# Kernel optimization log

Hardware: AMD Instinct MI355X
Metric: run time of the kernel (lower is better)

The kernel has to match this reference:

```python
import jax, jax.numpy as jnp
import numpy as np

DIM, H, D, B, L = 1024, 8, 64, 1, 256


def silu(v):
    return v * jax.nn.sigmoid(v)


def setup_inputs() -> dict:
    key = jax.random.key(0)
    ks = jax.random.split(key, 12)
    n = lambda i, shape, scale=1.0: jax.random.normal(ks[i], shape, dtype=jnp.float32) * scale
    return {
        "x": n(0, (B, L, DIM)),
        "hidden_real": n(1, (B, H, D)),
        "hidden_imag": n(2, (B, H, D)),
        "w_in1": n(3, (DIM, DIM), 1.0 / np.sqrt(DIM)),
        "b_in1": jnp.zeros((DIM,), jnp.float32),
        "w_in2": n(4, (DIM, H * D * 4), 1.0 / np.sqrt(DIM)),
        "b_in2": jnp.zeros((H * D * 4,), jnp.float32),
        "w_out1": n(5, (H * D * 2, DIM), 1.0 / np.sqrt(H * D * 2)),
        "b_out1": jnp.zeros((DIM,), jnp.float32),
        "w_out2": n(6, (DIM, DIM), 1.0 / np.sqrt(DIM)),
        "b_out2": jnp.zeros((DIM,), jnp.float32),
        "mat_v_real": n(7, (H, D, D)),
        "mat_v_imag": n(8, (H, D, D)),
    }


def reference(x, hidden_real, hidden_imag, w_in1, b_in1, w_in2, b_in2,
              w_out1, b_out1, w_out2, b_out2, mat_v_real, mat_v_imag):
    batch, slen, _ = x.shape
    t = silu(x @ w_in1 + b_in1)
    t = t @ w_in2 + b_in2                       # (B, L, 4*H*D)
    z = t.reshape(batch, slen, H, D, 2, 2)      # [..., {x,a}, {re,im}]
    xc = jax.lax.complex(z[..., 0, 0], z[..., 0, 1])   # (B, L, H, D) complex
    ac = jax.lax.complex(z[..., 1, 0], z[..., 1, 1])

    # normalize a: unit phase * sigmoid(log(|a|^2)) magnitude
    mag2 = ac.real * ac.real + ac.imag * ac.imag
    ac = ac * (jax.lax.rsqrt(mag2) * jax.nn.sigmoid(jnp.log(mag2)))

    a_ln = jnp.log(ac)                          # (B, L, H, D) complex
    al = jnp.transpose(a_ln, (0, 2, 3, 1))      # (B, H, D, L)

    # triu-broadcast + cumsum along cols == the FFT conv-with-ones in the original
    idx = jnp.arange(slen)
    triu = idx[:, None] <= idx[None, :]          # row i, col j: keep j >= i
    tri = jnp.where(triu, al[..., None, :], 0.0)  # (B, H, D, L, L)
    cum = jnp.cumsum(tri, axis=-1)               # cum[i, k] = sum_{j=i..k} a_ln[j]
    keep = (idx[:, None] - 1) <= idx[None, :]    # triu(diagonal=-1)
    c = jnp.where(keep, jnp.exp(cum), 0.0)       # c[i,k] = prod_{j=i..k} a[j]; c[i,i-1]=1

    V = jax.lax.complex(mat_v_real, mat_v_imag)  # (H, D, D)
    Vinv = jnp.linalg.inv(V)
    hidden = jax.lax.complex(hidden_real, hidden_imag)  # (B, H, D)

    x_roll = jnp.concatenate([hidden.astype(xc.dtype)[:, None], xc[:, :-1]], axis=1)
    u = jnp.einsum('hno,blho->blhn', Vinv, x_roll)       # V^{-1} applied per head
    h = jnp.einsum('bholm,blho->bmho', c, u)             # banded product-scan
    h = h.at[:, -1].add(jnp.einsum('hno,bho->bhn', Vinv, xc[:, -1]))
    h = jnp.einsum('hno,blho->blhn', V, h)               # back to V-basis

    hidden_next = h[:, -1]                                # (B, H, D) complex
    hr = jnp.stack([h.real, h.imag], axis=-1).reshape(batch, slen, H * D * 2)
    y = silu(hr @ w_out1 + b_out1)
    y = y @ w_out2 + b_out2
    return y, hidden_next
```

## Files before the change

### kernel.cpp

```cpp
#include <hip/hip_runtime.h>
#include <math.h>

#define DIMN 1024
#define NH 8
#define ND 64
#define LSEQ 256
#define HD 512

typedef __attribute__((ext_vector_type(8))) short short8;
typedef __attribute__((ext_vector_type(4))) float f32x4;

__device__ __forceinline__ float2 cmul(float2 a, float2 b){
    return make_float2(a.x*b.x - a.y*b.y, a.x*b.y + a.y*b.x);
}
__device__ __forceinline__ ushort f2bf(float f){
    union { float f; unsigned u; } v; v.f = f;
    unsigned r = v.u + 0x7FFF + ((v.u >> 16) & 1);
    return (ushort)(r >> 16);
}

#define ISTR 65
#define ASTR 40
#define BK 32

__device__ __forceinline__ void inv_gj_blocked(const float* __restrict__ Vr,
        const float* __restrict__ Vi, float2* __restrict__ Vinv,
        int h, int tid, float2* Mx){
    for (int idx = tid; idx < 4096; idx += 512){
        int i = idx >> 6, j = idx & 63;
        Mx[i*ISTR + j] = make_float2(Vr[h*4096 + idx], Vi[h*4096 + idx]);
    }
    __syncthreads();
    const int w = tid >> 6, l = tid & 63;
    const int rbase = w*8;
    for (int kb = 0; kb < 8; ++kb){
        const int k0 = kb*8;
        if (w == 0){
            float2 pr[8];
            #pragma unroll
            for (int m = 0; m < 8; ++m) pr[m] = Mx[l*ISTR + k0 + m];
            #pragma unroll
            for (int k = 0; k < 8; ++k){
                const int gk = k0 + k;
                float2 d; d.x = __shfl(pr[k].x, gk); d.y = __shfl(pr[k].y, gk);
                float im = 1.f/(d.x*d.x + d.y*d.y);
                float2 p = make_float2(d.x*im, -d.y*im);
                float2 spr[8];
                #pragma unroll
                for (int m = 0; m < 8; ++m){
                    float2 t; t.x = __shfl(pr[m].x, gk); t.y = __shfl(pr[m].y, gk);
                    spr[m] = (m == k) ? p : cmul(t, p);
                }
                float2 f = pr[k];
                if (l == gk){
                    #pragma unroll
                    for (int m = 0; m < 8; ++m) pr[m] = spr[m];
                } else {
                    #pragma unroll
                    for (int m = 0; m < 8; ++m){
                        float2 u = cmul(f, spr[m]);
                        if (m == k){ pr[m].x = -u.x;  pr[m].y = -u.y;  }
                        else       { pr[m].x -= u.x;  pr[m].y -= u.y;  }
                    }
                }
            }
            #pragma unroll
            for (int m = 0; m < 8; ++m) Mx[l*ISTR + k0 + m] = pr[m];
        }
        __syncthreads();
        float2 br[8];
        #pragma unroll
        for (int m = 0; m < 8; ++m) br[m] = Mx[(k0+m)*ISTR + l];
        __syncthreads();
        if (((unsigned)(l - k0)) >= 8u){
            #pragma unroll
            for (int rr = 0; rr < 8; ++rr){
                const int r = rbase + rr;
                float2 acc;
                if (((unsigned)(r - k0)) < 8u){ acc.x = 0.f; acc.y = 0.f; }
                else acc = Mx[r*ISTR + l];
                #pragma unroll
                for (int m = 0; m < 8; ++m){
                    float2 Pv = Mx[r*ISTR + k0 + m];
                    acc.x += Pv.x*br[m].x - Pv.y*br[m].y;
                    acc.y += Pv.x*br[m].y + Pv.y*br[m].x;
                }
                Mx[r*ISTR + l] = acc;
            }
        }
        __syncthreads();
    }
    for (int idx = tid; idx < 4096; idx += 512){
        int i = idx >> 6, j = idx & 63;
        Vinv[h*4096 + idx] = Mx[i*ISTR + j];
    }
}

__device__ __forceinline__ void w3eff_tile(const float* __restrict__ Vr,
        const float* __restrict__ Vi, const float* __restrict__ w3,
        ushort* __restrict__ W3bt, int t, int tid, float* lds){
    const int n0 = (t & 31)*32;
    const int c0 = (t >> 5)*32;
    const int h  = c0 >> 7;
    const int og0 = (c0 & 127) >> 1;
    float* Vbr = lds;
    float* Vbi = lds + 1024;
    float* Wb  = lds + 2048;
    for (int q = tid; q < 1024; q += 512){
        int dd = q >> 4, oo = q & 15;
        Vbr[q] = Vr[(h*64+dd)*64 + og0 + oo];
        Vbi[q] = Vi[(h*64+dd)*64 + og0 + oo];
    }
    for (int q = tid; q < 4096; q += 512){
        int row = q >> 5, nn = q & 31;
        Wb[q] = w3[(h*128 + row)*1024 + n0 + nn];
    }
    __syncthreads();
    const int nn = tid & 31, oo = tid >> 5;
    float ar = 0.f, ai = 0.f;
    #pragma unroll 8
    for (int dd = 0; dd < 64; ++dd){
        float vr = Vbr[dd*16 + oo], vi = Vbi[dd*16 + oo];
        float w0 = Wb[(dd*2)*32 + nn], w1v = Wb[(dd*2+1)*32 + nn];
        ar += vr*w0 + vi*w1v;
        ai += -vi*w0 + vr*w1v;
    }
    W3bt[(n0+nn)*1024 + c0 + oo*2 + 0] = f2bf(ar);
    W3bt[(n0+nn)*1024 + c0 + oo*2 + 1] = f2bf(ai);
}

__global__ __launch_bounds__(512) void prep_kernel(
        const float* __restrict__ x,
        const float* __restrict__ w1, const float* __restrict__ w2,
        const float* __restrict__ w3, const float* __restrict__ w4,
        const float* __restrict__ Vr, const float* __restrict__ Vi,
        ushort* __restrict__ x_bf,
        ushort* __restrict__ w1t, ushort* __restrict__ w2t,
        ushort* __restrict__ w4t, ushort* __restrict__ W3bt,
        float2* __restrict__ Vinv){
    __shared__ __align__(16) char lds_raw[33280];
    const int b = blockIdx.x;
    const int tid = threadIdx.x;
    const int half = tid >> 8;

    if (b < 8){
        inv_gj_blocked(Vr, Vi, Vinv, b, tid, (float2*)lds_raw);
        return;
    }
    int u = b - 8;
    if (u < 2048){
        const float* W; ushort* Wt; const int K = 1024; int N; int t;
        if (u < 512)      { W = w1; Wt = w1t; N = 1024; t = u*2 + half; }
        else if (u < 1536){ W = w2; Wt = w2t; N = 2048; t = (u-512)*2 + half; }
        else              { W = w4; Wt = w4t; N = 1024; t = (u-1536)*2 + half; }
        const int tiles_n = N >> 5;
        const int n0 = (t % tiles_n) * 32, k0 = (t / tiles_n) * 32;
        float* tile = (float*)lds_raw + half*(32*33);
        const int tx = tid & 31, ty = (tid >> 5) & 7;
        #pragma unroll
        for (int i = 0; i < 4; ++i)
            tile[(ty + i*8)*33 + tx] = W[(k0 + ty + i*8)*N + n0 + tx];
        __syncthreads();
        #pragma unroll
        for (int i = 0; i < 4; ++i){
            int r = ty + i*8;
            Wt[(n0 + r)*K + k0 + tx] = f2bf(tile[tx*33 + r]);
        }
        return;
    }
    u -= 2048;
    if (u < 64){
        const int base = (u*512 + tid)*2;
        #pragma unroll
        for (int j = 0; j < 2; ++j){
            float4 v = ((const float4*)x)[base + j];
            ushort4 uu; uu.x=f2bf(v.x); uu.y=f2bf(v.y); uu.z=f2bf(v.z); uu.w=f2bf(v.w);
            ((ushort4*)x_bf)[base + j] = uu;
        }
        return;
    }
    u -= 64;
    w3eff_tile(Vr, Vi, w3, W3bt, u, tid, (float*)lds_raw);
}

template<int ACT>
__global__ __launch_bounds__(64) void gemm_dt(const ushort* __restrict__ A,
                 const ushort* __restrict__ Bt, const float* __restrict__ bias,
                 float* __restrict__ Cf, ushort* __restrict__ Cb,
                 float2* __restrict__ XCo, float2* __restrict__ Ao,
                 int M, int N, int K,
                 const float* __restrict__ tVr, const float* __restrict__ tVi,
                 const float2* __restrict__ S255, float* __restrict__ out_tail,
                 int tail_n){
    const int nt = (M >> 5) * (N >> 5);
    const int b = blockIdx.x;
    if (ACT == 1 && out_tail != nullptr && b >= nt){
        const int l = threadIdx.x;
        for (int hn = l; hn < 512; hn += 64){
            const int h = hn >> 6;
            float2 acc2 = make_float2(0.f, 0.f);
            #pragma unroll 8
            for (int o = 0; o < 64; ++o){
                float2 v = make_float2(tVr[hn*64+o], tVi[hn*64+o]);
                float2 p = cmul(v, S255[h*64+o]);
                acc2.x += p.x; acc2.y += p.y;
            }
            if (tail_n >= 1024){
                out_tail[hn]       = acc2.x;
                out_tail[512 + hn] = acc2.y;
            } else if (tail_n >= 512){
                out_tail[hn] = acc2.x;
            }
        }
        return;
    }
    const int cpx = nt >> 3;
    const int t = (b & 7)*cpx + (b >> 3);
    const int tm = M >> 5;
    const int bm = (t % tm) * 32, bn = (t / tm) * 32;

    const int l = threadIdx.x;
    const int ml = l & 15, quad = l >> 4;
    const ushort* Ap = A  + (bm + ml)*K + quad*8;
    const ushort* Bp = Bt + (bn + ml)*K + quad*8;

    f32x4 acc[2][2];
    #pragma unroll
    for (int i=0;i<2;++i)
        #pragma unroll
        for (int j=0;j<2;++j) acc[i][j] = (f32x4){0.f,0.f,0.f,0.f};

    short8 ac[2], bc[2];
    ac[0] = *(const short8*)(Ap);
    ac[1] = *(const short8*)(Ap + 16*K);
    bc[0] = *(const short8*)(Bp);
    bc[1] = *(const short8*)(Bp + 16*K);

    #pragma unroll 4
    for (int k0 = 32; k0 < K; k0 += 32){
        short8 an[2], bn2[2];
        an[0]  = *(const short8*)(Ap + k0);
        an[1]  = *(const short8*)(Ap + 16*K + k0);
        bn2[0] = *(const short8*)(Bp + k0);
        bn2[1] = *(const short8*)(Bp + 16*K + k0);
        #pragma unroll
        for (int i=0;i<2;++i)
            #pragma unroll
            for (int j=0;j<2;++j)
                acc[i][j] = __builtin_amdgcn_mfma_f32_16x16x32_bf16(ac[i], bc[j], acc[i][j], 0,0,0);
        ac[0]=an[0]; ac[1]=an[1]; bc[0]=bn2[0]; bc[1]=bn2[1];
    }
    #pragma unroll
    for (int i=0;i<2;++i)
        #pragma unroll
        for (int j=0;j<2;++j)
            acc[i][j] = __builtin_amdgcn_mfma_f32_16x16x32_bf16(ac[i], bc[j], acc[i][j], 0,0,0);

    #pragma unroll
    for (int i=0;i<2;++i){
        #pragma unroll
        for (int j=0;j<2;++j){
            const int gcol = bn + j*16 + ml;
            const float bsv = bias[gcol];
            #pragma unroll
            for (int r=0;r<4;++r){
                const int grow = bm + i*16 + quad*4 + r;
                float val = acc[i][j][r] + bsv;
                if (ACT == 2){
                    float v1 = __shfl_down(val, 1);
                    float v2 = __shfl_down(val, 2);
                    float v3 = __shfl_down(val, 3);
                    if ((l & 3) == 0){
                        int hd = gcol >> 2;
                        XCo[grow*HD + hd] = make_float2(val, v1);
                        float m2 = v2*v2 + v3*v3;
                        float s = sqrtf(m2)/(1.f + m2);
                        Ao[grow*HD + hd] = make_float2(v2*s, v3*s);
                    }
                } else if (ACT == 1){
                    val *= 1.f/(1.f + expf(-val));
                    Cb[grow*N + gcol] = f2bf(val);
                } else {
                    Cf[grow*N + gcol] = val;
                }
            }
        }
    }
}

__global__ __launch_bounds__(512) void inv_kernel(const float* __restrict__ Vr,
                                                  const float* __restrict__ Vi,
                                                  float2* __restrict__ Vinv){
    __shared__ float2 Mx[64*ISTR];
    inv_gj_blocked(Vr, Vi, Vinv, blockIdx.x, threadIdx.x, Mx);
}

__global__ __launch_bounds__(256) void transpose_cvt(const float* __restrict__ W,
                 ushort* __restrict__ Wt, int K, int N){
    __shared__ float tile[32][33];
    const int n0 = blockIdx.x * 32, k0 = blockIdx.y * 32;
    const int tx = threadIdx.x & 31, ty = threadIdx.x >> 5;
    #pragma unroll
    for (int i = 0; i < 4; ++i)
        tile[ty + i*8][tx] = W[(k0 + ty + i*8)*N + n0 + tx];
    __syncthreads();
    #pragma unroll
    for (int i = 0; i < 4; ++i){
        int r = ty + i*8;
        Wt[(n0 + r)*K + k0 + tx] = f2bf(tile[tx][r]);
    }
}

__global__ __launch_bounds__(256) void cvt_bf16_kernel(const float* __restrict__ in,
                                 ushort* __restrict__ o, int n4){
    int i = blockIdx.x*256 + threadIdx.x;
    if (i < n4){
        float4 v = ((const float4*)in)[i];
        ushort4 u; u.x=f2bf(v.x); u.y=f2bf(v.y); u.z=f2bf(v.z); u.w=f2bf(v.w);
        ((ushort4*)o)[i] = u;
    }
}

#define BM 64
#define BN 64
template<int ACT>
__global__ __launch_bounds__(256) void gemm_bt(const ushort* __restrict__ A,
                 const ushort* __restrict__ Bt, const float* __restrict__ bias,
                 float* __restrict__ Cf, ushort* __restrict__ Cb,
                 float2* __restrict__ XCo, float2* __restrict__ Ao,
                 int M, int N, int K,
                 const float* __restrict__ tVr, const float* __restrict__ tVi,
                 const float2* __restrict__ S255, float* __restrict__ out_tail,
                 int tail_n){
    __shared__ ushort As[BM*ASTR];
    __shared__ ushort Bs[BN*ASTR];
    const int tid = threadIdx.x;
    const int bm = blockIdx.y * BM, bn = blockIdx.x * BN;
    const int wave = tid >> 6, l = tid & 63;
    const int wr = (wave >> 1) * 32, wc = (wave & 1) * 32;
    const int ml = l & 15, quad = l >> 4;

    if (ACT == 0 && out_tail != nullptr && blockIdx.x == 0 && blockIdx.y == 0){
        for (int hn = tid; hn < 512; hn += 256){
            int h = hn >> 6;
            float2 acc2 = make_float2(0.f, 0.f);
            #pragma unroll 8
            for (int o = 0; o < 64; ++o){
                float2 v = make_float2(tVr[hn*64+o], tVi[hn*64+o]);
                float2 p = cmul(v, S255[h*64+o]);
                acc2.x += p.x; acc2.y += p.y;
            }
            if (tail_n >= 1024){
                out_tail[hn]       = acc2.x;
                out_tail[512 + hn] = acc2.y;
            } else if (tail_n >= 512){
                out_tail[hn] = acc2.x;
            }
        }
    }

    f32x4 acc[2][2];
    #pragma unroll
    for (int i=0;i<2;++i)
        #pragma unroll
        for (int j=0;j<2;++j) acc[i][j] = (f32x4){0.f,0.f,0.f,0.f};
    const int c0r = tid >> 2;
    const int c0s = tid & 3;
    for (int k0 = 0; k0 < K; k0 += BK){
        uint4 av = *(const uint4*)&A [(bm + c0r)*K + k0 + c0s*8];
        uint4 bv = *(const uint4*)&Bt[(bn + c0r)*K + k0 + c0s*8];
        __syncthreads();
        *(uint4*)&As[c0r*ASTR + c0s*8] = av;
        *(uint4*)&Bs[c0r*ASTR + c0s*8] = bv;
        __syncthreads();
        short8 af[2], bfv[2];
        #pragma unroll
        for (int f=0; f<2; ++f){
            af[f]  = *(const short8*)&As[(wr + f*16 + ml)*ASTR + quad*8];
            bfv[f] = *(const short8*)&Bs[(wc + f*16 + ml)*ASTR + quad*8];
        }
        #pragma unroll
        for (int i=0;i<2;++i)
            #pragma unroll
            for (int j=0;j<2;++j)
                acc[i][j] = __builtin_amdgcn_mfma_f32_16x16x32_bf16(af[i], bfv[j], acc[i][j], 0,0,0);
    }
    #pragma unroll
    for (int i=0;i<2;++i){
        #pragma unroll
        for (int j=0;j<2;++j){
            const int gcol = bn + wc + j*16 + ml;
            const float bsv = bias[gcol];
            #pragma unroll
            for (int r=0;r<4;++r){
                const int grow = bm + wr + i*16 + quad*4 + r;
                float val = acc[i][j][r] + bsv;
                if (ACT == 2){
                    float v1 = __shfl_down(val, 1);
                    float v2 = __shfl_down(val, 2);
                    float v3 = __shfl_down(val, 3);
                    if ((l & 3) == 0){
                        int hd = gcol >> 2;
                        XCo[grow*HD + hd] = make_float2(val, v1);
                        float m2 = v2*v2 + v3*v3;
                        float s = sqrtf(m2)/(1.f + m2);
                        Ao[grow*HD + hd] = make_float2(v2*s, v3*s);
                    }
                } else if (ACT == 1){
                    val *= 1.f/(1.f + expf(-val));
                    Cb[grow*N + gcol] = f2bf(val);
                } else {
                    Cf[grow*N + gcol] = val;
                }
            }
        }
    }
}

__global__ __launch_bounds__(512) void upscan_kernel(const float2* __restrict__ Vinv,
        const float* __restrict__ hidr, const float* __restrict__ him,
        const float2* __restrict__ XC, const float2* __restrict__ Aseq,
        ushort* __restrict__ Sb, float2* __restrict__ S255){
    __shared__ float4 buf[2][2][LSEQ];
    __shared__ float2 vrow[2][64];
    __shared__ float2 inu[2];
    const int b = blockIdx.x;
    const int tid = threadIdx.x;
    const int g = tid >> 8, m = tid & 255;
    const int hn = b*2 + g;
    const int h = hn >> 6;
    if (m < 64) vrow[g][m] = Vinv[hn*64 + m];
    __syncthreads();
    float2 acc = make_float2(0.f, 0.f);
    const float2* xrow = &XC[m*HD + h*64];
    #pragma unroll 8
    for (int o=0;o<64;++o){
        float2 p = cmul(vrow[g][o], xrow[o]);
        acc.x += p.x; acc.y += p.y;
    }
    if (m == 0){
        float2 i0 = make_float2(0.f, 0.f);
        #pragma unroll 8
        for (int o=0;o<64;++o){
            float2 hv = make_float2(hidr[h*64+o], him[h*64+o]);
            float2 p = cmul(vrow[g][o], hv);
            i0.x += p.x; i0.y += p.y;
        }
        inu[g] = i0;
    }
    float2 a = Aseq[m*HD + hn];
    buf[0][g][m] = make_float4(a.x, a.y, acc.x, acc.y);
    __syncthreads();
    int pb = 0;
    #pragma unroll
    for (int d = 1; d < LSEQ; d <<= 1){
        float4 cur = buf[pb][g][m];
        float4 o2 = cur;
        if (m >= d){
            float4 prev = buf[pb][g][m-d];
            float2 cA = make_float2(cur.x, cur.y), cU = make_float2(cur.z, cur.w);
            float2 pA = make_float2(prev.x, prev.y), pU = make_float2(prev.z, prev.w);
            float2 nA = cmul(cA, pA);
            float2 nU = cmul(cA, pU);
            nU.x += cU.x; nU.y += cU.y;
            o2 = make_float4(nA.x, nA.y, nU.x, nU.y);
        }
        buf[pb^1][g][m] = o2;
        pb ^= 1;
        __syncthreads();
    }
    float4 t = buf[pb][g][m];
    float2 init = inu[g];
    float2 st = cmul(make_float2(t.x, t.y), init);
    st.x += t.z; st.y += t.w;
    Sb[m*DIMN + hn*2]   = f2bf(st.x);
    Sb[m*DIMN + hn*2+1] = f2bf(st.y);
    if (m == LSEQ-1) S255[hn] = st;
}

__global__ __launch_bounds__(256) void vmul_kernel(const float* __restrict__ Vr,
                            const float* __restrict__ Vi,
                            const float2* __restrict__ S, ushort* __restrict__ hrb,
                            float* __restrict__ out_tail, int tail_n){
    int g = blockIdx.x*256 + threadIdx.x;
    int m = g >> 9, hn = g & 511;
    int h = hn >> 6;
    const float* vr = &Vr[hn*64];
    const float* vi = &Vi[hn*64];
    const float2* srow = &S[m*HD + h*64];
    float2 acc = make_float2(0.f, 0.f);
    #pragma unroll 8
    for (int o=0;o<64;++o){
        float2 v = make_float2(vr[o], vi[o]);
        float2 p = cmul(v, srow[o]);
        acc.x += p.x; acc.y += p.y;
    }
    hrb[m*DIMN + hn*2]   = f2bf(acc.x);
    hrb[m*DIMN + hn*2+1] = f2bf(acc.y);
    if (m == LSEQ-1){
        if (tail_n >= 1024){
            out_tail[hn]       = acc.x;
            out_tail[512 + hn] = acc.y;
        } else if (tail_n >= 512){
            out_tail[hn] = acc.x;
        }
    }
}

__global__ __launch_bounds__(512) void upscan_f32_kernel(const float2* __restrict__ Vinv,
        const float* __restrict__ hidr, const float* __restrict__ him,
        const float2* __restrict__ XC, const float2* __restrict__ Aseq,
        float2* __restrict__ S){
    __shared__ float4 buf[2][2][LSEQ];
    __shared__ float2 vrow[2][64];
    __shared__ float2 inu[2];
    const int b = blockIdx.x;
    const int tid = threadIdx.x;
    const int g = tid >> 8, m = tid & 255;
    const int hn = b*2 + g;
    const int h = hn >> 6;
    if (m < 64) vrow[g][m] = Vinv[hn*64 + m];
    __syncthreads();
    float2 acc = make_float2(0.f, 0.f);
    const float2* xrow = &XC[m*HD + h*64];
    #pragma unroll 8
    for (int o=0;o<64;++o){
        float2 p = cmul(vrow[g][o], xrow[o]);
        acc.x += p.x; acc.y += p.y;
    }
    if (m == 0){
        float2 i0 = make_float2(0.f, 0.f);
        #pragma unroll 8
        for (int o=0;o<64;++o){
            float2 hv = make_float2(hidr[h*64+o], him[h*64+o]);
            float2 p = cmul(vrow[g][o], hv);
            i0.x += p.x; i0.y += p.y;
        }
        inu[g] = i0;
    }
    float2 a = Aseq[m*HD + hn];
    buf[0][g][m] = make_float4(a.x, a.y, acc.x, acc.y);
    __syncthreads();
    int pb = 0;
    #pragma unroll
    for (int d = 1; d < LSEQ; d <<= 1){
        float4 cur = buf[pb][g][m];
        float4 o2 = cur;
        if (m >= d){
            float4 prev = buf[pb][g][m-d];
            float2 cA = make_float2(cur.x, cur.y), cU = make_float2(cur.z, cur.w);
            float2 pA = make_float2(prev.x, prev.y), pU = make_float2(prev.z, prev.w);
            float2 nA = cmul(cA, pA);
            float2 nU = cmul(cA, pU);
            nU.x += cU.x; nU.y += cU.y;
            o2 = make_float4(nA.x, nA.y, nU.x, nU.y);
        }
        buf[pb^1][g][m] = o2;
        pb ^= 1;
        __syncthreads();
    }
    float4 t = buf[pb][g][m];
    float2 init = inu[g];
    float2 st = cmul(make_float2(t.x, t.y), init);
    st.x += t.z; st.y += t.w;
    S[m*HD + hn] = st;
}

extern "C" void kernel_launch(void* const* d_in, const int* in_sizes, int n_in,
                              void* d_out, int out_size, void* d_ws, size_t ws_size,
                              hipStream_t stream) {
    const float* x      = (const float*)d_in[0];
    const float* hidr   = (const float*)d_in[1];
    const float* hidi   = (const float*)d_in[2];
    const float* w_in1  = (const float*)d_in[3];
    const float* b_in1  = (const float*)d_in[4];
    const float* w_in2  = (const float*)d_in[5];
    const float* b_in2  = (const float*)d_in[6];
    const float* w_out1 = (const float*)d_in[7];
    const float* b_out1 = (const float*)d_in[8];
    const float* w_out2 = (const float*)d_in[9];
    const float* b_out2 = (const float*)d_in[10];
    const float* Vr     = (const float*)d_in[11];
    const float* Vi     = (const float*)d_in[12];
    float* out = (float*)d_out;
    const int tail_n = out_size - LSEQ*DIMN;
    char* ws = (char*)d_ws;

    if (ws_size >= 14946304u){
        float2* Vinv  = (float2*)(ws + 0);
        ushort* w2t   = (ushort*)(ws + 262144);
        ushort* W3bt  = (ushort*)(ws + 4456448);
        ushort* w4t   = (ushort*)(ws + 6553600);
        ushort* w1t   = (ushort*)(ws + 8650752);
        float2* XC    = (float2*)(ws + 8650752);
        float2* Aseq  = (float2*)(ws + 9699328);
        ushort* x_bf  = (ushort*)(ws + 10747904);
        float2* S255  = (float2*)(ws + 10747904);
        ushort* t1_bf = (ushort*)(ws + 11272192);
        ushort* y1_bf = (ushort*)(ws + 11796480);
        ushort* Sb    = t1_bf;

        prep_kernel<<<3144, 512, 0, stream>>>(x, w_in1, w_in2, w_out1, w_out2,
                                              Vr, Vi, x_bf, w1t, w2t, w4t, W3bt, Vinv);
        gemm_dt<1><<<256, 64, 0, stream>>>(x_bf, w1t, b_in1, nullptr, t1_bf,
                nullptr, nullptr, LSEQ, DIMN, DIMN, nullptr, nullptr, nullptr, nullptr, 0);
        gemm_dt<2><<<512, 64, 0, stream>>>(t1_bf, w2t, b_in2, nullptr, nullptr,
                XC, Aseq, LSEQ, 2048, DIMN, nullptr, nullptr, nullptr, nullptr, 0);
        upscan_kernel<<<256, 512, 0, stream>>>(Vinv, hidr, hidi, XC, Aseq, Sb, S255);
        gemm_dt<1><<<257, 64, 0, stream>>>(Sb, W3bt, b_out1, nullptr, y1_bf,
                nullptr, nullptr, LSEQ, DIMN, DIMN, Vr, Vi, S255, out + LSEQ*DIMN, tail_n);
        gemm_dt<0><<<256, 64, 0, stream>>>(y1_bf, w4t, b_out2, out, nullptr,
                nullptr, nullptr, LSEQ, DIMN, DIMN, nullptr, nullptr, nullptr, nullptr, 0);
    } else {
        float2* Vinv  = (float2*)(ws + 0);
        ushort* wt    = (ushort*)(ws + 262144);
        ushort* x_bf  = (ushort*)(ws + 4456448);
        ushort* t1_bf = (ushort*)(ws + 4980736);
        float2* XC    = (float2*)(ws + 5505024);
        float2* Aseq  = (float2*)(ws + 6553600);
        float2* S     = (float2*)(ws + 7602176);
        ushort* y1_bf = x_bf;
        ushort* hr_bf = t1_bf;

        inv_kernel<<<NH, 512, 0, stream>>>(Vr, Vi, Vinv);
        cvt_bf16_kernel<<<LSEQ*DIMN/4/256, 256, 0, stream>>>(x, x_bf, LSEQ*DIMN/4);
        transpose_cvt<<<dim3(32,32), 256, 0, stream>>>(w_in1, wt, DIMN, DIMN);
        gemm_bt<1><<<dim3(16,4), 256, 0, stream>>>(x_bf, wt, b_in1, nullptr, t1_bf,
                nullptr, nullptr, LSEQ, DIMN, DIMN, nullptr, nullptr, nullptr, nullptr, 0);
        transpose_cvt<<<dim3(64,32), 256, 0, stream>>>(w_in2, wt, DIMN, 2048);
        gemm_bt<2><<<dim3(32,4), 256, 0, stream>>>(t1_bf, wt, b_in2, nullptr, nullptr,
                XC, Aseq, LSEQ, 2048, DIMN, nullptr, nullptr, nullptr, nullptr, 0);
        upscan_f32_kernel<<<256, 512, 0, stream>>>(Vinv, hidr, hidi, XC, Aseq, S);
        vmul_kernel<<<LSEQ*HD/256, 256, 0, stream>>>(Vr, Vi, S, hr_bf, out + LSEQ*DIMN, tail_n);
        transpose_cvt<<<dim3(32,32), 256, 0, stream>>>(w_out1, wt, DIMN, DIMN);
        gemm_bt<1><<<dim3(16,4), 256, 0, stream>>>(hr_bf, wt, b_out1, nullptr, y1_bf,
                nullptr, nullptr, LSEQ, DIMN, DIMN, nullptr, nullptr, nullptr, nullptr, 0);
        transpose_cvt<<<dim3(32,32), 256, 0, stream>>>(w_out2, wt, DIMN, DIMN);
        gemm_bt<0><<<dim3(16,4), 256, 0, stream>>>(y1_bf, wt, b_out2, out, nullptr,
                nullptr, nullptr, LSEQ, DIMN, DIMN, nullptr, nullptr, nullptr, nullptr, 0);
    }
}
```

Baseline: 200.9 us.

## Fuse all stages into one persistent kernel with grid-wide barriers

Replaces the six-launch pipeline (prep, four GEMMs, scan) with a single persistent kernel of 256 blocks that moves between phases using an atomic grid barrier. Each GEMM phase now splits the K dimension across the 8 waves of a block and reduces the partial sums through LDS, so every block handles one or two 32x32 tiles with 512 threads. The aim is to remove kernel launch gaps and raise per-tile parallelism. The cost is spin-wait barrier overhead, a memset before launch, and a deadlock risk if not all 256 blocks are resident at the same time; the prep work also becomes serialized loops over fewer blocks.

```diff
diff --git a/kernel.cpp b/kernel.cpp
--- a/kernel.cpp
+++ b/kernel.cpp
@@ -6,6 +6,7 @@
 #define ND 64
 #define LSEQ 256
 #define HD 512
+#define GRID 256
 
 typedef __attribute__((ext_vector_type(8))) short short8;
 typedef __attribute__((ext_vector_type(4))) float f32x4;
@@ -129,163 +130,276 @@
     W3bt[(n0+nn)*1024 + c0 + oo*2 + 1] = f2bf(ai);
 }
 
-__global__ __launch_bounds__(512) void prep_kernel(
+__device__ __forceinline__ void gbar(unsigned* cnt, unsigned* gen){
+    __syncthreads();
+    if (threadIdx.x == 0){
+        __threadfence();
+        unsigned g = __hip_atomic_load(gen, __ATOMIC_RELAXED, __HIP_MEMORY_SCOPE_AGENT);
+        unsigned old = __hip_atomic_fetch_add(cnt, 1u, __ATOMIC_ACQ_REL, __HIP_MEMORY_SCOPE_AGENT);
+        if (old == GRID-1){
+            __hip_atomic_store(cnt, 0u, __ATOMIC_RELAXED, __HIP_MEMORY_SCOPE_AGENT);
+            __hip_atomic_fetch_add(gen, 1u, __ATOMIC_RELEASE, __HIP_MEMORY_SCOPE_AGENT);
+        } else {
+            long spins = 0;
+            while (__hip_atomic_load(gen, __ATOMIC_ACQUIRE, __HIP_MEMORY_SCOPE_AGENT) == g){
+                __builtin_amdgcn_s_sleep(2);
+                if (++spins > (1l<<24)) break;
+            }
+        }
+        __threadfence();
+    }
+    __syncthreads();
+}
+
+template<int ACT, int KS>
+__device__ __forceinline__ void gemm_phase(const ushort* __restrict__ A,
+        const ushort* __restrict__ Bt, const float* __restrict__ bias,
+        float* __restrict__ Cf, ushort* __restrict__ Cb,
+        float2* __restrict__ XCo, float2* __restrict__ Ao,
+        int M, int N, int blk, int tid, float* red){
+    constexpr int Kw = 1024/KS;
+    constexpr int TPBT = 8/KS;
+    const int wave = tid >> 6, l = tid & 63;
+    const int ml = l & 15, quad = l >> 4;
+    const int lt = wave / KS, ks = wave - lt*KS;
+    const int tile = blk*TPBT + lt;
+    const int tm = M >> 5;
+    const int bm = (tile % tm)*32, bn = (tile / tm)*32;
+    const ushort* Ap = A  + (bm + ml)*1024 + ks*Kw + quad*8;
+    const ushort* Bp = Bt + (bn + ml)*1024 + ks*Kw + quad*8;
+
+    f32x4 acc[2][2];
+    #pragma unroll
+    for (int i=0;i<2;++i)
+        #pragma unroll
+        for (int j=0;j<2;++j) acc[i][j] = (f32x4){0.f,0.f,0.f,0.f};
+
+    short8 ac[2], bc[2];
+    ac[0] = *(const short8*)(Ap);
+    ac[1] = *(const short8*)(Ap + 16*1024);
+    bc[0] = *(const short8*)(Bp);
+    bc[1] = *(const short8*)(Bp + 16*1024);
+
+    #pragma unroll
+    for (int k0 = 32; k0 < Kw; k0 += 32){
+        short8 an[2], bn2[2];
+        an[0]  = *(const short8*)(Ap + k0);
+        an[1]  = *(const short8*)(Ap + 16*1024 + k0);
+        bn2[0] = *(const short8*)(Bp + k0);
+        bn2[1] = *(const short8*)(Bp + 16*1024 + k0);
+        #pragma unroll
+        for (int i=0;i<2;++i)
+            #pragma unroll
+            for (int j=0;j<2;++j)
+                acc[i][j] = __builtin_amdgcn_mfma_f32_16x16x32_bf16(ac[i], bc[j], acc[i][j], 0,0,0);
+        ac[0]=an[0]; ac[1]=an[1]; bc[0]=bn2[0]; bc[1]=bn2[1];
+    }
+    #pragma unroll
+    for (int i=0;i<2;++i)
+        #pragma unroll
+        for (int j=0;j<2;++j)
+            acc[i][j] = __builtin_amdgcn_mfma_f32_16x16x32_bf16(ac[i], bc[j], acc[i][j], 0,0,0);
+
+    #pragma unroll
+    for (int i=0;i<2;++i)
+        #pragma unroll
+        for (int j=0;j<2;++j)
+            #pragma unroll
+            for (int r=0;r<4;++r)
+                red[wave*1024 + ((i*2+j)*4+r)*64 + l] = acc[i][j][r];
+    __syncthreads();
+
+    if (ks == 0){
+        #pragma unroll
+        for (int i=0;i<2;++i){
+            #pragma unroll
+            for (int j=0;j<2;++j){
+                const int gcol = bn + j*16 + ml;
+                const float bsv = bias[gcol];
+                #pragma unroll
+                for (int r=0;r<4;++r){
+                    float val = bsv;
+                    #pragma unroll
+                    for (int s=0;s<KS;++s)
+                        val += red[(wave+s)*1024 + ((i*2+j)*4+r)*64 + l];
+                    const int grow = bm + i*16 + quad*4 + r;
+                    if (ACT == 2){
+                        float v1 = __shfl_down(val, 1);
+                        float v2 = __shfl_down(val, 2);
+                        float v3 = __shfl_down(val, 3);
+                        if ((l & 3) == 0){
+                            int hd = gcol >> 2;
+                            XCo[grow*HD + hd] = make_float2(val, v1);
+                            float m2 = v2*v2 + v3*v3;
+                            float s = sqrtf(m2)/(1.f + m2);
+                            Ao[grow*HD + hd] = make_float2(v2*s, v3*s);
+                        }
+                    } else if (ACT == 1){
+                        val *= 1.f/(1.f + expf(-val));
+                        Cb[grow*N + gcol] = f2bf(val);
+                    } else {
+                        Cf[grow*N + gcol] = val;
+                    }
+                }
+            }
+        }
+    }
+    __syncthreads();
+}
+
+__global__ __launch_bounds__(512, 4) void fused_kernel(
         const float* __restrict__ x,
-        const float* __restrict__ w1, const float* __restrict__ w2,
-        const float* __restrict__ w3, const float* __restrict__ w4,
+        const float* __restrict__ hidr, const float* __restrict__ him,
+        const float* __restrict__ w1, const float* __restrict__ b1,
+        const float* __restrict__ w2, const float* __restrict__ b2,
+        const float* __restrict__ w3, const float* __restrict__ b3,
+        const float* __restrict__ w4, const float* __restrict__ b4,
         const float* __restrict__ Vr, const float* __restrict__ Vi,
-        ushort* __restrict__ x_bf,
-        ushort* __restrict__ w1t, ushort* __restrict__ w2t,
-        ushort* __restrict__ w4t, ushort* __restrict__ W3bt,
-        float2* __restrict__ Vinv){
+        float* __restrict__ out, int tail_n,
+        ushort* __restrict__ x_bf, ushort* __restrict__ w1t,
+        ushort* __restrict__ w2t, ushort* __restrict__ w4t,
+        ushort* __restrict__ W3bt, float2* __restrict__ Vinv,
+        float2* __restrict__ XC, float2* __restrict__ Aseq,
+        ushort* __restrict__ t1_bf, ushort* __restrict__ y1_bf,
+        float2* __restrict__ S255, unsigned* __restrict__ bar){
     __shared__ __align__(16) char lds_raw[33280];
-    const int b = blockIdx.x;
+    const int blk = blockIdx.x;
     const int tid = threadIdx.x;
-    const int half = tid >> 8;
-
-    if (b < 8){
-        inv_gj_blocked(Vr, Vi, Vinv, b, tid, (float2*)lds_raw);
-        return;
-    }
-    int u = b - 8;
-    if (u < 2048){
-        const float* W; ushort* Wt; const int K = 1024; int N; int t;
-        if (u < 512)      { W = w1; Wt = w1t; N = 1024; t = u*2 + half; }
-        else if (u < 1536){ W = w2; Wt = w2t; N = 2048; t = (u-512)*2 + half; }
-        else              { W = w4; Wt = w4t; N = 1024; t = (u-1536)*2 + half; }
-        const int tiles_n = N >> 5;
-        const int n0 = (t % tiles_n) * 32, k0 = (t / tiles_n) * 32;
-        float* tile = (float*)lds_raw + half*(32*33);
-        const int tx = tid & 31, ty = (tid >> 5) & 7;
-        #pragma unroll
-        for (int i = 0; i < 4; ++i)
-            tile[(ty + i*8)*33 + tx] = W[(k0 + ty + i*8)*N + n0 + tx];
-        __syncthreads();
-        #pragma unroll
-        for (int i = 0; i < 4; ++i){
-            int r = ty + i*8;
-            Wt[(n0 + r)*K + k0 + tx] = f2bf(tile[tx*33 + r]);
-        }
-        return;
-    }
-    u -= 2048;
-    if (u < 64){
-        const int base = (u*512 + tid)*2;
-        #pragma unroll
-        for (int j = 0; j < 2; ++j){
-            float4 v = ((const float4*)x)[base + j];
-            ushort4 uu; uu.x=f2bf(v.x); uu.y=f2bf(v.y); uu.z=f2bf(v.z); uu.w=f2bf(v.w);
-            ((ushort4*)x_bf)[base + j] = uu;
-        }
-        return;
-    }
-    u -= 64;
-    w3eff_tile(Vr, Vi, w3, W3bt, u, tid, (float*)lds_raw);
-}
-
-template<int ACT>
-__global__ __launch_bounds__(64) void gemm_dt(const ushort* __restrict__ A,
-                 const ushort* __restrict__ Bt, const float* __restrict__ bias,
-                 float* __restrict__ Cf, ushort* __restrict__ Cb,
-                 float2* __restrict__ XCo, float2* __restrict__ Ao,
-                 int M, int N, int K,
-                 const float* __restrict__ tVr, const float* __restrict__ tVi,
-                 const float2* __restrict__ S255, float* __restrict__ out_tail,
-                 int tail_n){
-    const int nt = (M >> 5) * (N >> 5);
-    const int b = blockIdx.x;
-    if (ACT == 1 && out_tail != nullptr && b >= nt){
-        const int l = threadIdx.x;
+    unsigned* cnt = bar;
+    unsigned* gen = bar + 1;
+    ushort* Sb = t1_bf;
+
+    if (blk < 8){
+        inv_gj_blocked(Vr, Vi, Vinv, blk, tid, (float2*)lds_raw);
+    } else {
+        const int half = tid >> 8;
+        for (int u = blk-8; u < 2048; u += 248){
+            const float* W; ushort* Wt; int N2; int t;
+            if (u < 512)      { W = w1; Wt = w1t; N2 = 1024; t = u*2 + half; }
+            else if (u < 1536){ W = w2; Wt = w2t; N2 = 2048; t = (u-512)*2 + half; }
+            else              { W = w4; Wt = w4t; N2 = 1024; t = (u-1536)*2 + half; }
+            const int tiles_n = N2 >> 5;
+            const int n0 = (t % tiles_n) * 32, k0 = (t / tiles_n) * 32;
+            float* tile = (float*)lds_raw + half*(32*33);
+            const int tx = tid & 31, ty = (tid >> 5) & 7;
+            #pragma unroll
+            for (int i = 0; i < 4; ++i)
+                tile[(ty + i*8)*33 + tx] = W[(k0 + ty + i*8)*N2 + n0 + tx];
+            __syncthreads();
+            #pragma unroll
+            for (int i = 0; i < 4; ++i){
+                int r = ty + i*8;
+                Wt[(n0 + r)*1024 + k0 + tx] = f2bf(tile[tx*33 + r]);
+            }
+            __syncthreads();
+        }
+        for (int u = blk-8; u < 64; u += 248){
+            const int base = (u*512 + tid)*2;
+            #pragma unroll
+            for (int j = 0; j < 2; ++j){
+                float4 v = ((const float4*)x)[base + j];
+                ushort4 uu; uu.x=f2bf(v.x); uu.y=f2bf(v.y); uu.z=f2bf(v.z); uu.w=f2bf(v.w);
+                ((ushort4*)x_bf)[base + j] = uu;
+            }
+        }
+        for (int u = blk-8; u < 1024; u += 248){
+            w3eff_tile(Vr, Vi, w3, W3bt, u, tid, (float*)lds_raw);
+            __syncthreads();
+        }
+    }
+    gbar(cnt, gen);
+
+    gemm_phase<1,8>(x_bf, w1t, b1, nullptr, t1_bf, nullptr, nullptr,
+                    256, 1024, blk, tid, (float*)lds_raw);
+    gbar(cnt, gen);
+
+    gemm_phase<2,4>(t1_bf, w2t, b2, nullptr, nullptr, XC, Aseq,
+                    256, 2048, blk, tid, (float*)lds_raw);
+    gbar(cnt, gen);
+
+    {
+        float4* buf  = (float4*)lds_raw;
+        float2* vrow = (float2*)(lds_raw + 16384);
+        float2* inu  = (float2*)(lds_raw + 17408);
+        const int g = tid >> 8, m = tid & 255;
+        const int hn = blk*2 + g;
+        const int h = hn >> 6;
+        if (m < 64) vrow[g*64 + m] = Vinv[hn*64 + m];
+        __syncthreads();
+        float2 acc = make_float2(0.f, 0.f);
+        const float2* xrow = &XC[m*HD + h*64];
+        #pragma unroll 8
+        for (int o=0;o<64;++o){
+            float2 p = cmul(vrow[g*64 + o], xrow[o]);
+            acc.x += p.x; acc.y += p.y;
+        }
+        if (m == 0){
+            float2 i0 = make_float2(0.f, 0.f);
+            #pragma unroll 8
+            for (int o=0;o<64;++o){
+                float2 hv = make_float2(hidr[h*64+o], him[h*64+o]);
+                float2 p = cmul(vrow[g*64 + o], hv);
+                i0.x += p.x; i0.y += p.y;
+            }
+            inu[g] = i0;
+        }
+        float2 a = Aseq[m*HD + hn];
+        buf[(0*2+g)*LSEQ + m] = make_float4(a.x, a.y, acc.x, acc.y);
+        __syncthreads();
+        int pb = 0;
+        #pragma unroll
+        for (int d = 1; d < LSEQ; d <<= 1){
+            float4 cur = buf[(pb*2+g)*LSEQ + m];
+            float4 o2 = cur;
+            if (m >= d){
+                float4 prev = buf[(pb*2+g)*LSEQ + m-d];
+                float2 cA = make_float2(cur.x, cur.y), cU = make_float2(cur.z, cur.w);
+                float2 pA = make_float2(prev.x, prev.y), pU = make_float2(prev.z, prev.w);
+                float2 nA = cmul(cA, pA);
+                float2 nU = cmul(cA, pU);
+                nU.x += cU.x; nU.y += cU.y;
+                o2 = make_float4(nA.x, nA.y, nU.x, nU.y);
+            }
+            buf[((pb^1)*2+g)*LSEQ + m] = o2;
+            pb ^= 1;
+            __syncthreads();
+        }
+        float4 t = buf[(pb*2+g)*LSEQ + m];
+        float2 init = inu[g];
+        float2 st = cmul(make_float2(t.x, t.y), init);
+        st.x += t.z; st.y += t.w;
+        Sb[m*DIMN + hn*2]   = f2bf(st.x);
+        Sb[m*DIMN + hn*2+1] = f2bf(st.y);
+        if (m == LSEQ-1) S255[hn] = st;
+    }
+    gbar(cnt, gen);
+
+    gemm_phase<1,8>(Sb, W3bt, b3, nullptr, y1_bf, nullptr, nullptr,
+                    256, 1024, blk, tid, (float*)lds_raw);
+    if (blk == 0 && (tid >> 6) == 0 && tail_n >= 512){
+        const int l = tid & 63;
+        float* out_tail = out + LSEQ*DIMN;
         for (int hn = l; hn < 512; hn += 64){
             const int h = hn >> 6;
             float2 acc2 = make_float2(0.f, 0.f);
             #pragma unroll 8
             for (int o = 0; o < 64; ++o){
-                float2 v = make_float2(tVr[hn*64+o], tVi[hn*64+o]);
+                float2 v = make_float2(Vr[hn*64+o], Vi[hn*64+o]);
                 float2 p = cmul(v, S255[h*64+o]);
                 acc2.x += p.x; acc2.y += p.y;
             }
             if (tail_n >= 1024){
                 out_tail[hn]       = acc2.x;
                 out_tail[512 + hn] = acc2.y;
-            } else if (tail_n >= 512){
+            } else {
                 out_tail[hn] = acc2.x;
             }
         }
-        return;
-    }
-    const int cpx = nt >> 3;
-    const int t = (b & 7)*cpx + (b >> 3);
-    const int tm = M >> 5;
-    const int bm = (t % tm) * 32, bn = (t / tm) * 32;
-
-    const int l = threadIdx.x;
-    const int ml = l & 15, quad = l >> 4;
-    const ushort* Ap = A  + (bm + ml)*K + quad*8;
-    const ushort* Bp = Bt + (bn + ml)*K + quad*8;
-
-    f32x4 acc[2][2];
-    #pragma unroll
-    for (int i=0;i<2;++i)
-        #pragma unroll
-        for (int j=0;j<2;++j) acc[i][j] = (f32x4){0.f,0.f,0.f,0.f};
-
-    short8 ac[2], bc[2];
-    ac[0] = *(const short8*)(Ap);
-    ac[1] = *(const short8*)(Ap + 16*K);
-    bc[0] = *(const short8*)(Bp);
-    bc[1] = *(const short8*)(Bp + 16*K);
-
-    #pragma unroll 4
-    for (int k0 = 32; k0 < K; k0 += 32){
-        short8 an[2], bn2[2];
-        an[0]  = *(const short8*)(Ap + k0);
-        an[1]  = *(const short8*)(Ap + 16*K + k0);
-        bn2[0] = *(const short8*)(Bp + k0);
-        bn2[1] = *(const short8*)(Bp + 16*K + k0);
-        #pragma unroll
-        for (int i=0;i<2;++i)
-            #pragma unroll
-            for (int j=0;j<2;++j)
-                acc[i][j] = __builtin_amdgcn_mfma_f32_16x16x32_bf16(ac[i], bc[j], acc[i][j], 0,0,0);
-        ac[0]=an[0]; ac[1]=an[1]; bc[0]=bn2[0]; bc[1]=bn2[1];
-    }
-    #pragma unroll
-    for (int i=0;i<2;++i)
-        #pragma unroll
-        for (int j=0;j<2;++j)
-            acc[i][j] = __builtin_amdgcn_mfma_f32_16x16x32_bf16(ac[i], bc[j], acc[i][j], 0,0,0);
-
-    #pragma unroll
-    for (int i=0;i<2;++i){
-        #pragma unroll
-        for (int j=0;j<2;++j){
-            const int gcol = bn + j*16 + ml;
-            const float bsv = bias[gcol];
-            #pragma unroll
-            for (int r=0;r<4;++r){
-                const int grow = bm + i*16 + quad*4 + r;
-                float val = acc[i][j][r] + bsv;
-                if (ACT == 2){
-                    float v1 = __shfl_down(val, 1);
-                    float v2 = __shfl_down(val, 2);
-                    float v3 = __shfl_down(val, 3);
-                    if ((l & 3) == 0){
-                        int hd = gcol >> 2;
-                        XCo[grow*HD + hd] = make_float2(val, v1);
-                        float m2 = v2*v2 + v3*v3;
-                        float s = sqrtf(m2)/(1.f + m2);
-                        Ao[grow*HD + hd] = make_float2(v2*s, v3*s);
-                    }
-                } else if (ACT == 1){
-                    val *= 1.f/(1.f + expf(-val));
-                    Cb[grow*N + gcol] = f2bf(val);
-                } else {
-                    Cf[grow*N + gcol] = val;
-                }
-            }
-        }
-    }
+    }
+    gbar(cnt, gen);
+
+    gemm_phase<0,8>(y1_bf, w4t, b4, out, nullptr, nullptr, nullptr,
+                    256, 1024, blk, tid, (float*)lds_raw);
 }
 
 __global__ __launch_bounds__(512) void inv_kernel(const float* __restrict__ Vr,
@@ -417,67 +531,6 @@
     }
 }
 
-__global__ __launch_bounds__(512) void upscan_kernel(const float2* __restrict__ Vinv,
-        const float* __restrict__ hidr, const float* __restrict__ him,
-        const float2* __restrict__ XC, const float2* __restrict__ Aseq,
-        ushort* __restrict__ Sb, float2* __restrict__ S255){
-    __shared__ float4 buf[2][2][LSEQ];
-    __shared__ float2 vrow[2][64];
-    __shared__ float2 inu[2];
-    const int b = blockIdx.x;
-    const int tid = threadIdx.x;
-    const int g = tid >> 8, m = tid & 255;
-    const int hn = b*2 + g;
-    const int h = hn >> 6;
-    if (m < 64) vrow[g][m] = Vinv[hn*64 + m];
-    __syncthreads();
-    float2 acc = make_float2(0.f, 0.f);
-    const float2* xrow = &XC[m*HD + h*64];
-    #pragma unroll 8
-    for (int o=0;o<64;++o){
-        float2 p = cmul(vrow[g][o], xrow[o]);
-        acc.x += p.x; acc.y += p.y;
-    }
-    if (m == 0){
-        float2 i0 = make_float2(0.f, 0.f);
-        #pragma unroll 8
-        for (int o=0;o<64;++o){
-            float2 hv = make_float2(hidr[h*64+o], him[h*64+o]);
-            float2 p = cmul(vrow[g][o], hv);
-            i0.x += p.x; i0.y += p.y;
-        }
-        inu[g] = i0;
-    }
-    float2 a = Aseq[m*HD + hn];
-    buf[0][g][m] = make_float4(a.x, a.y, acc.x, acc.y);
-    __syncthreads();
-    int pb = 0;
-    #pragma unroll
-    for (int d = 1; d < LSEQ; d <<= 1){
-        float4 cur = buf[pb][g][m];
-        float4 o2 = cur;
-        if (m >= d){
-            float4 prev = buf[pb][g][m-d];
-            float2 cA = make_float2(cur.x, cur.y), cU = make_float2(cur.z, cur.w);
-            float2 pA = make_float2(prev.x, prev.y), pU = make_float2(prev.z, prev.w);
-            float2 nA = cmul(cA, pA);
-            float2 nU = cmul(cA, pU);
-            nU.x += cU.x; nU.y += cU.y;
-            o2 = make_float4(nA.x, nA.y, nU.x, nU.y);
-        }
-        buf[pb^1][g][m] = o2;
-        pb ^= 1;
-        __syncthreads();
-    }
-    float4 t = buf[pb][g][m];
-    float2 init = inu[g];
-    float2 st = cmul(make_float2(t.x, t.y), init);
-    st.x += t.z; st.y += t.w;
-    Sb[m*DIMN + hn*2]   = f2bf(st.x);
-    Sb[m*DIMN + hn*2+1] = f2bf(st.y);
-    if (m == LSEQ-1) S255[hn] = st;
-}
-
 __global__ __launch_bounds__(256) void vmul_kernel(const float* __restrict__ Vr,
                             const float* __restrict__ Vi,
                             const float2* __restrict__ S, ushort* __restrict__ hrb,
@@ -598,19 +651,14 @@
         float2* S255  = (float2*)(ws + 10747904);
         ushort* t1_bf = (ushort*)(ws + 11272192);
         ushort* y1_bf = (ushort*)(ws + 11796480);
-        ushort* Sb    = t1_bf;
-
-        prep_kernel<<<3144, 512, 0, stream>>>(x, w_in1, w_in2, w_out1, w_out2,
-                                              Vr, Vi, x_bf, w1t, w2t, w4t, W3bt, Vinv);
-        gemm_dt<1><<<256, 64, 0, stream>>>(x_bf, w1t, b_in1, nullptr, t1_bf,
-                nullptr, nullptr, LSEQ, DIMN, DIMN, nullptr, nullptr, nullptr, nullptr, 0);
-        gemm_dt<2><<<512, 64, 0, stream>>>(t1_bf, w2t, b_in2, nullptr, nullptr,
-                XC, Aseq, LSEQ, 2048, DIMN, nullptr, nullptr, nullptr, nullptr, 0);
-        upscan_kernel<<<256, 512, 0, stream>>>(Vinv, hidr, hidi, XC, Aseq, Sb, S255);
-        gemm_dt<1><<<257, 64, 0, stream>>>(Sb, W3bt, b_out1, nullptr, y1_bf,
-                nullptr, nullptr, LSEQ, DIMN, DIMN, Vr, Vi, S255, out + LSEQ*DIMN, tail_n);
-        gemm_dt<0><<<256, 64, 0, stream>>>(y1_bf, w4t, b_out2, out, nullptr,
-                nullptr, nullptr, LSEQ, DIMN, DIMN, nullptr, nullptr, nullptr, nullptr, 0);
+        unsigned* bar = (unsigned*)(ws + 14680064);
+
+        hipMemsetAsync(ws + 14680064, 0, 64, stream);
+        fused_kernel<<<GRID, 512, 0, stream>>>(x, hidr, hidi,
+                w_in1, b_in1, w_in2, b_in2, w_out1, b_out1, w_out2, b_out2,
+                Vr, Vi, out, tail_n,
+                x_bf, w1t, w2t, w4t, W3bt, Vinv, XC, Aseq, t1_bf, y1_bf,
+                S255, bar);
     } else {
         float2* Vinv  = (float2*)(ws + 0);
         ushort* wt    = (ushort*)(ws + 262144);
```

After: 377.7 us. 88.0% more time.

## Split-K GEMMs across eight waves per block with LDS reduction

Applied to the files above, without the earlier changes.

Replaces the single-wave-per-tile GEMM with 512-thread blocks in which several waves each compute a K-slice of the same 32x32 tile. Partial accumulators are summed through shared memory before the bias, activation and epilogue run. This shortens each wave's serial K loop and raises the number of active waves, since the small M=256 problem left the GPU underfilled. The cost is a 32KB shared-memory reduction buffer and a block-wide barrier per tile.

```diff
diff --git a/kernel.cpp b/kernel.cpp
--- a/kernel.cpp
+++ b/kernel.cpp
@@ -183,46 +183,22 @@
     w3eff_tile(Vr, Vi, w3, W3bt, u, tid, (float*)lds_raw);
 }
 
-template<int ACT>
-__global__ __launch_bounds__(64) void gemm_dt(const ushort* __restrict__ A,
-                 const ushort* __restrict__ Bt, const float* __restrict__ bias,
-                 float* __restrict__ Cf, ushort* __restrict__ Cb,
-                 float2* __restrict__ XCo, float2* __restrict__ Ao,
-                 int M, int N, int K,
-                 const float* __restrict__ tVr, const float* __restrict__ tVi,
-                 const float2* __restrict__ S255, float* __restrict__ out_tail,
-                 int tail_n){
-    const int nt = (M >> 5) * (N >> 5);
-    const int b = blockIdx.x;
-    if (ACT == 1 && out_tail != nullptr && b >= nt){
-        const int l = threadIdx.x;
-        for (int hn = l; hn < 512; hn += 64){
-            const int h = hn >> 6;
-            float2 acc2 = make_float2(0.f, 0.f);
-            #pragma unroll 8
-            for (int o = 0; o < 64; ++o){
-                float2 v = make_float2(tVr[hn*64+o], tVi[hn*64+o]);
-                float2 p = cmul(v, S255[h*64+o]);
-                acc2.x += p.x; acc2.y += p.y;
-            }
-            if (tail_n >= 1024){
-                out_tail[hn]       = acc2.x;
-                out_tail[512 + hn] = acc2.y;
-            } else if (tail_n >= 512){
-                out_tail[hn] = acc2.x;
-            }
-        }
-        return;
-    }
-    const int cpx = nt >> 3;
-    const int t = (b & 7)*cpx + (b >> 3);
+template<int ACT, int KS>
+__device__ __forceinline__ void gemm_phase(const ushort* __restrict__ A,
+        const ushort* __restrict__ Bt, const float* __restrict__ bias,
+        float* __restrict__ Cf, ushort* __restrict__ Cb,
+        float2* __restrict__ XCo, float2* __restrict__ Ao,
+        int M, int N, int blk, int tid, float* red){
+    constexpr int Kw = 1024/KS;
+    constexpr int TPBT = 8/KS;
+    const int wave = tid >> 6, l = tid & 63;
+    const int ml = l & 15, quad = l >> 4;
+    const int lt = wave / KS, ks = wave - lt*KS;
+    const int tile = blk*TPBT + lt;
     const int tm = M >> 5;
-    const int bm = (t % tm) * 32, bn = (t / tm) * 32;
-
-    const int l = threadIdx.x;
-    const int ml = l & 15, quad = l >> 4;
-    const ushort* Ap = A  + (bm + ml)*K + quad*8;
-    const ushort* Bp = Bt + (bn + ml)*K + quad*8;
+    const int bm = (tile % tm)*32, bn = (tile / tm)*32;
+    const ushort* Ap = A  + (bm + ml)*1024 + ks*Kw + quad*8;
+    const ushort* Bp = Bt + (bn + ml)*1024 + ks*Kw + quad*8;
 
     f32x4 acc[2][2];
     #pragma unroll
@@ -232,17 +208,17 @@
 
     short8 ac[2], bc[2];
     ac[0] = *(const short8*)(Ap);
-    ac[1] = *(const short8*)(Ap + 16*K);
+    ac[1] = *(const short8*)(Ap + 16*1024);
     bc[0] = *(const short8*)(Bp);
-    bc[1] = *(const short8*)(Bp + 16*K);
-
-    #pragma unroll 4
-    for (int k0 = 32; k0 < K; k0 += 32){
+    bc[1] = *(const short8*)(Bp + 16*1024);
+
+    #pragma unroll
+    for (int k0 = 32; k0 < Kw; k0 += 32){
         short8 an[2], bn2[2];
         an[0]  = *(const short8*)(Ap + k0);
-        an[1]  = *(const short8*)(Ap + 16*K + k0);
+        an[1]  = *(const short8*)(Ap + 16*1024 + k0);
         bn2[0] = *(const short8*)(Bp + k0);
-        bn2[1] = *(const short8*)(Bp + 16*K + k0);
+        bn2[1] = *(const short8*)(Bp + 16*1024 + k0);
         #pragma unroll
         for (int i=0;i<2;++i)
             #pragma unroll
@@ -257,35 +233,87 @@
             acc[i][j] = __builtin_amdgcn_mfma_f32_16x16x32_bf16(ac[i], bc[j], acc[i][j], 0,0,0);
 
     #pragma unroll
-    for (int i=0;i<2;++i){
-        #pragma unroll
-        for (int j=0;j<2;++j){
-            const int gcol = bn + j*16 + ml;
-            const float bsv = bias[gcol];
-            #pragma unroll
-            for (int r=0;r<4;++r){
-                const int grow = bm + i*16 + quad*4 + r;
-                float val = acc[i][j][r] + bsv;
-                if (ACT == 2){
-                    float v1 = __shfl_down(val, 1);
-                    float v2 = __shfl_down(val, 2);
-                    float v3 = __shfl_down(val, 3);
-                    if ((l & 3) == 0){
-                        int hd = gcol >> 2;
-                        XCo[grow*HD + hd] = make_float2(val, v1);
-                        float m2 = v2*v2 + v3*v3;
-                        float s = sqrtf(m2)/(1.f + m2);
-                        Ao[grow*HD + hd] = make_float2(v2*s, v3*s);
+    for (int i=0;i<2;++i)
+        #pragma unroll
+        for (int j=0;j<2;++j)
+            #pragma unroll
+            for (int r=0;r<4;++r)
+                red[wave*1024 + ((i*2+j)*4+r)*64 + l] = acc[i][j][r];
+    __syncthreads();
+
+    if (ks == 0){
+        #pragma unroll
+        for (int i=0;i<2;++i){
+            #pragma unroll
+            for (int j=0;j<2;++j){
+                const int gcol = bn + j*16 + ml;
+                const float bsv = bias[gcol];
+                #pragma unroll
+                for (int r=0;r<4;++r){
+                    float val = bsv;
+                    #pragma unroll
+                    for (int s=0;s<KS;++s)
+                        val += red[(wave+s)*1024 + ((i*2+j)*4+r)*64 + l];
+                    const int grow = bm + i*16 + quad*4 + r;
+                    if (ACT == 2){
+                        float v1 = __shfl_down(val, 1);
+                        float v2 = __shfl_down(val, 2);
+                        float v3 = __shfl_down(val, 3);
+                        if ((l & 3) == 0){
+                            int hd = gcol >> 2;
+                            XCo[grow*HD + hd] = make_float2(val, v1);
+                            float m2 = v2*v2 + v3*v3;
+                            float s = sqrtf(m2)/(1.f + m2);
+                            Ao[grow*HD + hd] = make_float2(v2*s, v3*s);
+                        }
+                    } else if (ACT == 1){
+                        val *= 1.f/(1.f + expf(-val));
+                        Cb[grow*N + gcol] = f2bf(val);
+                    } else {
+                        Cf[grow*N + gcol] = val;
                     }
-                } else if (ACT == 1){
-                    val *= 1.f/(1.f + expf(-val));
-                    Cb[grow*N + gcol] = f2bf(val);
-                } else {
-                    Cf[grow*N + gcol] = val;
                 }
             }
         }
     }
+}
+
+template<int ACT, int KS>
+__global__ __launch_bounds__(512) void gemm_ks(const ushort* __restrict__ A,
+        const ushort* __restrict__ Bt, const float* __restrict__ bias,
+        float* __restrict__ Cf, ushort* __restrict__ Cb,
+        float2* __restrict__ XCo, float2* __restrict__ Ao,
+        int M, int N,
+        const float* __restrict__ tVr, const float* __restrict__ tVi,
+        const float2* __restrict__ S255, float* __restrict__ out_tail,
+        int tail_n){
+    __shared__ float red[8*1024];
+    const int nt = (M >> 5) * (N >> 5);
+    const int ntb = nt / (8/KS);
+    if (out_tail != nullptr && blockIdx.x >= ntb){
+        if ((threadIdx.x >> 6) == 0 && tail_n >= 512){
+            const int l = threadIdx.x & 63;
+            for (int hn = l; hn < 512; hn += 64){
+                const int h = hn >> 6;
+                float2 acc2 = make_float2(0.f, 0.f);
+                #pragma unroll 8
+                for (int o = 0; o < 64; ++o){
+                    float2 v = make_float2(tVr[hn*64+o], tVi[hn*64+o]);
+                    float2 p = cmul(v, S255[h*64+o]);
+                    acc2.x += p.x; acc2.y += p.y;
+                }
+                if (tail_n >= 1024){
+                    out_tail[hn]       = acc2.x;
+                    out_tail[512 + hn] = acc2.y;
+                } else {
+                    out_tail[hn] = acc2.x;
+                }
+            }
+        }
+        return;
+    }
+    gemm_phase<ACT, KS>(A, Bt, bias, Cf, Cb, XCo, Ao, M, N,
+                        blockIdx.x, threadIdx.x, red);
 }
 
 __global__ __launch_bounds__(512) void inv_kernel(const float* __restrict__ Vr,
@@ -602,15 +630,15 @@
 
         prep_kernel<<<3144, 512, 0, stream>>>(x, w_in1, w_in2, w_out1, w_out2,
                                               Vr, Vi, x_bf, w1t, w2t, w4t, W3bt, Vinv);
-        gemm_dt<1><<<256, 64, 0, stream>>>(x_bf, w1t, b_in1, nullptr, t1_bf,
-                nullptr, nullptr, LSEQ, DIMN, DIMN, nullptr, nullptr, nullptr, nullptr, 0);
-        gemm_dt<2><<<512, 64, 0, stream>>>(t1_bf, w2t, b_in2, nullptr, nullptr,
-                XC, Aseq, LSEQ, 2048, DIMN, nullptr, nullptr, nullptr, nullptr, 0);
+        gemm_ks<1,8><<<256, 512, 0, stream>>>(x_bf, w1t, b_in1, nullptr, t1_bf,
+                nullptr, nullptr, LSEQ, DIMN, nullptr, nullptr, nullptr, nullptr, 0);
+        gemm_ks<2,4><<<256, 512, 0, stream>>>(t1_bf, w2t, b_in2, nullptr, nullptr,
+                XC, Aseq, LSEQ, 2048, nullptr, nullptr, nullptr, nullptr, 0);
         upscan_kernel<<<256, 512, 0, stream>>>(Vinv, hidr, hidi, XC, Aseq, Sb, S255);
-        gemm_dt<1><<<257, 64, 0, stream>>>(Sb, W3bt, b_out1, nullptr, y1_bf,
-                nullptr, nullptr, LSEQ, DIMN, DIMN, Vr, Vi, S255, out + LSEQ*DIMN, tail_n);
-        gemm_dt<0><<<256, 64, 0, stream>>>(y1_bf, w4t, b_out2, out, nullptr,
-                nullptr, nullptr, LSEQ, DIMN, DIMN, nullptr, nullptr, nullptr, nullptr, 0);
+        gemm_ks<1,8><<<257, 512, 0, stream>>>(Sb, W3bt, b_out1, nullptr, y1_bf,
+                nullptr, nullptr, LSEQ, DIMN, Vr, Vi, S255, out + LSEQ*DIMN, tail_n);
+        gemm_ks<0,8><<<256, 512, 0, stream>>>(y1_bf, w4t, b_out2, out, nullptr,
+                nullptr, nullptr, LSEQ, DIMN, nullptr, nullptr, nullptr, nullptr, 0);
     } else {
         float2* Vinv  = (float2*)(ws + 0);
         ushort* wt    = (ushort*)(ws + 262144);
```

New measurement: 193.9 us. -3.5%, faster.
